# Kernel optimization log

Hardware: AMD Instinct MI355X
Metric: run time of the kernel (lower is better)

The kernel has to match this reference:

```python
import jax, jax.numpy as jnp
import numpy as np
import math

D_MODEL = 1024
N_HEADS = 16
FFN_DIM = 4096
B, L = 8, 1024
LN_EPS = 1e-5


def setup_inputs() -> dict:
    key = jax.random.key(0)
    ks = jax.random.split(key, 16)
    s = 1.0 / math.sqrt(D_MODEL)
    sf = 1.0 / math.sqrt(FFN_DIM)
    # weights stored [in, out] (transposed vs torch nn.Linear)
    return {
        "x": jax.random.normal(ks[0], (B, L, D_MODEL), dtype=jnp.float32),
        "Wq": jax.random.normal(ks[1], (D_MODEL, D_MODEL), dtype=jnp.float32) * s,
        "bq": jnp.zeros((D_MODEL,), jnp.float32),
        "Wk": jax.random.normal(ks[2], (D_MODEL, D_MODEL), dtype=jnp.float32) * s,
        "bk": jnp.zeros((D_MODEL,), jnp.float32),
        "Wv": jax.random.normal(ks[3], (D_MODEL, D_MODEL), dtype=jnp.float32) * s,
        "bv": jnp.zeros((D_MODEL,), jnp.float32),
        "Wo": jax.random.normal(ks[4], (D_MODEL, D_MODEL), dtype=jnp.float32) * s,
        "bo": jnp.zeros((D_MODEL,), jnp.float32),
        "W1": jax.random.normal(ks[5], (D_MODEL, FFN_DIM), dtype=jnp.float32) * s,
        "b1": jnp.zeros((FFN_DIM,), jnp.float32),
        "W2": jax.random.normal(ks[6], (FFN_DIM, D_MODEL), dtype=jnp.float32) * sf,
        "b2": jnp.zeros((D_MODEL,), jnp.float32),
        "gamma": jnp.ones((D_MODEL,), jnp.float32),
        "beta": jnp.zeros((D_MODEL,), jnp.float32),
    }


def reference(x, Wq, bq, Wk, bk, Wv, bv, Wo, bo, W1, b1, W2, b2, gamma, beta):
    Bb, Ll, D = x.shape
    H = N_HEADS
    E = D // H
    scale = 1.0 / math.sqrt(E)
    # multi-head attention (dropout is identity in eval)
    q = (x @ Wq + bq).reshape(Bb, Ll, H, E)
    k = (x @ Wk + bk).reshape(Bb, Ll, H, E)
    v = (x @ Wv + bv).reshape(Bb, Ll, H, E)
    scores = jnp.einsum('blhe,bshe->bhls', q, k)  # [B,H,L,L]
    A = jax.nn.softmax(scale * scores, axis=-1)
    ctx = jnp.einsum('bhls,bshd->blhd', A, v).reshape(Bb, Ll, D)
    attn_out = ctx @ Wo + bo
    x = x + attn_out
    # FFN: conv1d kernel_size=1 == pointwise linear; exact (erf) GELU as in F.gelu
    h = jax.nn.gelu(x @ W1 + b1, approximate=False)
    x = x + (h @ W2 + b2)
    # LayerNorm
    mu = jnp.mean(x, axis=-1, keepdims=True)
    var = jnp.mean(jnp.square(x - mu), axis=-1, keepdims=True)
    out = (x - mu) * jax.lax.rsqrt(var + LN_EPS) * gamma + beta
    return out
```

## Files before the change

### kernel.cpp

```cpp
#include <hip/hip_runtime.h>
#include <cmath>

typedef __attribute__((ext_vector_type(8))) _Float16 half8;
typedef __attribute__((ext_vector_type(4))) _Float16 half4;
typedef __attribute__((ext_vector_type(4))) float f32x4;

__device__ __forceinline__ void glds16(const void* g, void* l) {
  __builtin_amdgcn_global_load_lds(
      (__attribute__((address_space(1))) const void*)g,
      (__attribute__((address_space(3))) void*)l, 16, 0, 0);
}

__global__ __launch_bounds__(256) void k_cvt(const float* __restrict__ in,
                                             _Float16* __restrict__ out) {
  int i = (blockIdx.x * 256 + threadIdx.x) * 8;
  const f32x4* p = (const f32x4*)(in + i);
  f32x4 a = p[0], b = p[1];
  half8 h;
  h[0] = (_Float16)a[0]; h[1] = (_Float16)a[1]; h[2] = (_Float16)a[2]; h[3] = (_Float16)a[3];
  h[4] = (_Float16)b[0]; h[5] = (_Float16)b[1]; h[6] = (_Float16)b[2]; h[7] = (_Float16)b[3];
  *(half8*)(out + i) = h;
}

__global__ __launch_bounds__(256) void k_wt(const float* __restrict__ W,
                                            _Float16* __restrict__ Wt, int K, int N) {
  __shared__ float t[32][33];
  int x = threadIdx.x & 31, y4 = (threadIdx.x >> 5) << 2;
  int n0 = blockIdx.x << 5, k0 = blockIdx.y << 5;
#pragma unroll
  for (int r = 0; r < 4; ++r) t[y4 + r][x] = W[(size_t)(k0 + y4 + r) * N + n0 + x];
  __syncthreads();
#pragma unroll
  for (int r = 0; r < 4; ++r) Wt[(size_t)(n0 + y4 + r) * K + k0 + x] = (_Float16)t[x][y4 + r];
}

__global__ void k_biascat(const float* __restrict__ a, const float* __restrict__ b,
                          const float* __restrict__ c, float* __restrict__ o) {
  int i = blockIdx.x * 256 + threadIdx.x;
  const float* s = i < 1024 ? a : (i < 2048 ? b : c);
  o[i] = s[i & 1023];
}

template <int BM, int EPI>
__global__ __launch_bounds__(512, 2) void k_gemm8(
    const _Float16* __restrict__ A, const _Float16* __restrict__ Bt,
    const float* __restrict__ bias, const float* __restrict__ res,
    float* __restrict__ outf, _Float16* __restrict__ outh, int M, int N, int K) {
  constexpr int MR = BM / 32;
  constexpr int MH2 = MR / 2;
  constexpr int AL = BM * 64;
  constexpr int BL = 256 * 64;
  constexpr int ABYTES = BM * 128;
  constexpr int BBYTES = 256 * 128;
  constexpr int AB2 = 2 * ABYTES;
  __shared__ _Float16 lds[2 * (AL + BL)];
  const char* ldsc = (const char*)lds;

  const int tid = threadIdx.x;
  const int lane = tid & 63;
  const int w = tid >> 6, wr = w >> 2, wc = w & 3;
  const int l15 = lane & 15, grp = lane >> 4;

  const int gx = gridDim.x;
  const int nwg = gx * gridDim.y;
  const int lid = blockIdx.y * gx + blockIdx.x;
  const int wid = (lid & 7) * (nwg >> 3) + (lid >> 3);
  const int m0 = (wid / gx) * BM, n0 = (wid % gx) * 256;

  const int m2 = (l15 >> 2) & 1, m01 = l15 & 3;
  const int chunk0 = (m2 << 2) | (grp ^ m01);
  const int aoff0 = wr * 2048 + l15 * 128 + chunk0 * 16;
  const int aoff1 = aoff0 ^ 64;
  const int boff0 = wc * 2048 + l15 * 128 + chunk0 * 16;
  const int boff1 = boff0 ^ 64;

  const int srow = tid >> 3;
  const int scs8 = ((tid & 7) ^ (srow & 7)) * 8;
  const int NK = K >> 6;

  f32x4 acc[MR][4] = {};
  half8 af[MH2][2], bf[2][2];

#define STG_A(J, MHH, KN)                                                      \
  _Pragma("unroll") for (int s = 0; s < BM / 128; ++s)                         \
      glds16(A + (size_t)(m0 + (MHH) * (BM / 2) + s * 64 + srow) * K +         \
                 (size_t)(KN)*64 + scs8,                                       \
             lds + (J)*AL + ((MHH) * (BM / 2) + s * 64) * 64 + tid * 8);
#define STG_B(J, NHH, KN)                                                      \
  _Pragma("unroll") for (int s = 0; s < 2; ++s)                                \
      glds16(Bt + (size_t)(n0 + (NHH)*128 + s * 64 + srow) * K +               \
                  (size_t)(KN)*64 + scs8,                                      \
             lds + 2 * AL + (J)*BL + ((NHH)*128 + s * 64) * 64 + tid * 8);

#define VM_P1                                                                  \
  do {                                                                         \
    if constexpr (BM == 256) asm volatile("s_waitcnt vmcnt(4)" ::: "memory");  \
    else asm volatile("s_waitcnt vmcnt(2)" ::: "memory");                      \
  } while (0)
#define VM_P2                                                                  \
  do {                                                                         \
    if constexpr (BM == 256) asm volatile("s_waitcnt vmcnt(4)" ::: "memory");  \
    else asm volatile("s_waitcnt vmcnt(3)" ::: "memory");                      \
  } while (0)
#define VM_P3                                                                  \
  do {                                                                         \
    if constexpr (BM == 256) asm volatile("s_waitcnt vmcnt(4)" ::: "memory");  \
  } while (0)
#define VM_P4 VM_P2

#define PHASE(J, MHQ, NHQ, RA, RB, STGSTMT, VMSTMT)                            \
  {                                                                            \
    if constexpr (RA) {                                                        \
      _Pragma("unroll") for (int i = 0; i < MH2; ++i) {                        \
        af[i][0] = *(const half8*)(ldsc + (J)*ABYTES +                         \
                                   ((MHQ)*MH2 + i) * 4096 + aoff0);            \
        af[i][1] = *(const half8*)(ldsc + (J)*ABYTES +                         \
                                   ((MHQ)*MH2 + i) * 4096 + aoff1);            \
      }                                                                        \
    }                                                                          \
    if constexpr (RB) {                                                        \
      _Pragma("unroll") for (int n = 0; n < 2; ++n) {                          \
        bf[n][0] = *(const half8*)(ldsc + AB2 + (J)*BBYTES +                   \
                                   ((NHQ)*2 + n) * 8192 + boff0);              \
        bf[n][1] = *(const half8*)(ldsc + AB2 + (J)*BBYTES +                   \
                                   ((NHQ)*2 + n) * 8192 + boff1);              \
      }                                                                        \
    }                                                                          \
    STGSTMT;                                                                   \
    __builtin_amdgcn_s_barrier();                                              \
    asm volatile("s_waitcnt lgkmcnt(0)" ::: "memory");                         \
    __builtin_amdgcn_sched_barrier(0);                                         \
    __builtin_amdgcn_s_setprio(1);                                             \
    _Pragma("unroll") for (int ks = 0; ks < 2; ++ks)                           \
        _Pragma("unroll") for (int i = 0; i < MH2; ++i)                        \
            _Pragma("unroll") for (int n = 0; n < 2; ++n)                      \
                acc[(MHQ)*MH2 + i][(NHQ)*2 + n] =                              \
                    __builtin_amdgcn_mfma_f32_16x16x32_f16(                    \
                        af[i][ks], bf[n][ks], acc[(MHQ)*MH2 + i][(NHQ)*2 + n], \
                        0, 0, 0);                                              \
    __builtin_amdgcn_s_setprio(0);                                             \
    VMSTMT;                                                                    \
    __builtin_amdgcn_s_barrier();                                              \
  }

#define KTILE(J, KT)                                                           \
  {                                                                            \
    const int kn_ = ((KT) + 1 < NK) ? (KT) + 1 : (KT);                         \
    PHASE(J, 0, 0, true, true, STG_A(1 - (J), 0, kn_), VM_P1)                  \
    PHASE(J, 0, 1, false, true, STG_B(1 - (J), 0, kn_), VM_P2)                 \
    PHASE(J, 1, 1, true, false, STG_B(1 - (J), 1, kn_), VM_P3)                 \
    PHASE(J, 1, 0, false, true, STG_A(1 - (J), 1, kn_), VM_P4)                 \
  }

  STG_A(0, 0, 0) STG_B(0, 0, 0) STG_B(0, 1, 0) STG_A(0, 1, 0)
  if constexpr (BM == 256) asm volatile("s_waitcnt vmcnt(4)" ::: "memory");
  else asm volatile("s_waitcnt vmcnt(3)" ::: "memory");
  __builtin_amdgcn_s_barrier();

#pragma unroll 1
  for (int kt = 0; kt < NK; kt += 2) {
    KTILE(0, kt)
    KTILE(1, kt + 1)
  }
  asm volatile("s_waitcnt vmcnt(0)" ::: "memory");
#undef KTILE
#undef PHASE
#undef VM_P1
#undef VM_P2
#undef VM_P3
#undef VM_P4
#undef STG_A
#undef STG_B

  float bcol[4];
#pragma unroll
  for (int n = 0; n < 4; ++n) bcol[n] = bias[n0 + (n * 4 + wc) * 16 + l15];
#pragma unroll
  for (int m = 0; m < MR; ++m) {
#pragma unroll
    for (int rr = 0; rr < 4; ++rr) {
      const size_t row = m0 + (m * 2 + wr) * 16 + grp * 4 + rr;
#pragma unroll
      for (int n = 0; n < 4; ++n) {
        const int col = n0 + (n * 4 + wc) * 16 + l15;
        float v = acc[m][n][rr] + bcol[n];
        const size_t idx = row * N + col;
        if (EPI == 0) {
          outh[idx] = (_Float16)v;
        } else if (EPI == 1) {
          float t2 = v + res[idx];
          outf[idx] = t2;
          outh[idx] = (_Float16)t2;
        } else if (EPI == 2) {
          float g = 0.5f * v * (1.0f + erff(v * 0.70710678118654752f));
          outh[idx] = (_Float16)g;
        } else {
          outf[idx] = v + res[idx];
        }
      }
    }
  }
}

__global__ __launch_bounds__(256) void k_vt(const _Float16* __restrict__ qkv,
                                            _Float16* __restrict__ Vt) {
  __shared__ _Float16 t[64 * 66];
  const int tid = threadIdx.x;
  const int bh = blockIdx.y, b = bh >> 4, h = bh & 15;
  const int s0 = blockIdx.x << 6;
#pragma unroll
  for (int p = 0; p < 2; ++p) {
    int lin = p * 256 + tid;
    int s = lin >> 3, c8 = lin & 7;
    half8 v = *(const half8*)&qkv[(size_t)(b * 1024 + s0 + s) * 3072 + 2048 + h * 64 + c8 * 8];
    union { half8 h8; unsigned u[4]; } u;
    u.h8 = v;
    unsigned* d = (unsigned*)&t[s * 66 + c8 * 8];
#pragma unroll
    for (int k = 0; k < 4; ++k) d[k] = u.u[k];
  }
  __syncthreads();
#pragma unroll
  for (int p = 0; p < 2; ++p) {
    int lin = p * 256 + tid;
    int e = lin >> 3, c8 = lin & 7;
    half8 v;
#pragma unroll
    for (int j = 0; j < 8; ++j) v[j] = t[(c8 * 8 + j) * 66 + e];
    *(half8*)&Vt[(size_t)(bh * 64 + e) * 1024 + s0 + c8 * 8] = v;
  }
}

__global__ __launch_bounds__(256) void k_attn(const _Float16* __restrict__ qkv,
                                              const _Float16* __restrict__ Vt,
                                              _Float16* __restrict__ ctx) {
  __shared__ _Float16 Ks[128 * 64];
  __shared__ _Float16 Vs[64 * 128];
  __shared__ _Float16 Ps[4][16 * 136];
  const int tid = threadIdx.x;
  const int lane = tid & 63, w = tid >> 6;
  const int l15 = lane & 15, grp = lane >> 4;
  const int bh = blockIdx.y, b = bh >> 4, h = bh & 15;
  const int q0 = blockIdx.x << 6;
  const float CSC = 0.125f * 1.44269504088896f;

  half8 qf[2];
  {
    const _Float16* qp = qkv + (size_t)(b * 1024 + q0 + w * 16 + l15) * 3072 + h * 64 + grp * 8;
    qf[0] = *(const half8*)qp;
    qf[1] = *(const half8*)(qp + 32);
  }
  f32x4 octx[4] = {};
  float mrun = -1e30f, lrun = 0.f;

  for (int kt = 0; kt < 8; ++kt) {
    const int s0 = kt * 128;
#pragma unroll
    for (int i = 0; i < 4; ++i) {
      {
        int srow = i * 32 + (tid >> 3);
        int c8 = (tid & 7) ^ (srow & 7);
        glds16(qkv + (size_t)(b * 1024 + s0 + srow) * 3072 + 1024 + h * 64 + c8 * 8,
               Ks + w * 512 + i * 2048);
      }
      {
        int erow = i * 16 + (tid >> 4);
        int c16 = (tid & 15) ^ (erow & 7);
        glds16(Vt + (size_t)(bh * 64 + erow) * 1024 + s0 + c16 * 8,
               Vs + w * 512 + i * 2048);
      }
    }
    __syncthreads();
    f32x4 sacc[8] = {};
#pragma unroll
    for (int ks = 0; ks < 2; ++ks)
#pragma unroll
      for (int f = 0; f < 8; ++f) {
        int srow = f * 16 + l15;
        half8 kf = *(const half8*)&Ks[srow * 64 + ((ks * 32 + grp * 8) ^ ((srow & 7) * 8))];
        sacc[f] = __builtin_amdgcn_mfma_f32_16x16x32_f16(kf, qf[ks], sacc[f], 0, 0, 0);
      }
    float sv[8][4];
    float tmax = -1e30f;
#pragma unroll
    for (int f = 0; f < 8; ++f)
#pragma unroll
      for (int r = 0; r < 4; ++r) {
        float v = sacc[f][r] * CSC;
        sv[f][r] = v;
        tmax = fmaxf(tmax, v);
      }
    tmax = fmaxf(tmax, __shfl_xor(tmax, 16));
    tmax = fmaxf(tmax, __shfl_xor(tmax, 32));
    float mnew = fmaxf(mrun, tmax);
    float corr = exp2f(mrun - mnew);
    float tsum = 0.f;
#pragma unroll
    for (int f = 0; f < 8; ++f)
#pragma unroll
      for (int r = 0; r < 4; ++r) {
        float pv = exp2f(sv[f][r] - mnew);
        sv[f][r] = pv;
        tsum += pv;
      }
    tsum += __shfl_xor(tsum, 16);
    tsum += __shfl_xor(tsum, 32);
    lrun = lrun * corr + tsum;
    mrun = mnew;
#pragma unroll
    for (int r = 0; r < 4; ++r) {
      float cq = __shfl(corr, (lane & 48) + grp * 4 + r);
#pragma unroll
      for (int jf = 0; jf < 4; ++jf) octx[jf][r] *= cq;
    }
#pragma unroll
    for (int f = 0; f < 8; ++f) {
      half4 pk;
      pk[0] = (_Float16)sv[f][0]; pk[1] = (_Float16)sv[f][1];
      pk[2] = (_Float16)sv[f][2]; pk[3] = (_Float16)sv[f][3];
      *(half4*)&Ps[w][l15 * 136 + f * 16 + grp * 4] = pk;
    }
#pragma unroll
    for (int ks2 = 0; ks2 < 4; ++ks2) {
      half8 pa = *(const half8*)&Ps[w][l15 * 136 + ks2 * 32 + grp * 8];
#pragma unroll
      for (int jf = 0; jf < 4; ++jf) {
        int erow = jf * 16 + l15;
        half8 vb = *(const half8*)&Vs[erow * 128 + ((ks2 * 32 + grp * 8) ^ ((erow & 7) * 8))];
        octx[jf] = __builtin_amdgcn_mfma_f32_16x16x32_f16(pa, vb, octx[jf], 0, 0, 0);
      }
    }
    __syncthreads();
  }
#pragma unroll
  for (int r = 0; r < 4; ++r) {
    float lq = __shfl(lrun, (lane & 48) + grp * 4 + r);
    float inv = 1.0f / lq;
    const size_t row = b * 1024 + q0 + w * 16 + grp * 4 + r;
#pragma unroll
    for (int jf = 0; jf < 4; ++jf)
      ctx[row * 1024 + h * 64 + jf * 16 + l15] = (_Float16)(octx[jf][r] * inv);
  }
}

__global__ __launch_bounds__(256) void k_ln(const float* xin, const float* __restrict__ gamma,
                                            const float* __restrict__ beta, float* out) {
  __shared__ float red[8];
  const int tid = threadIdx.x;
  const size_t row = blockIdx.x;
  f32x4 v = *(const f32x4*)&xin[row * 1024 + tid * 4];
  float s = v[0] + v[1] + v[2] + v[3];
  float s2 = v[0] * v[0] + v[1] * v[1] + v[2] * v[2] + v[3] * v[3];
#pragma unroll
  for (int o = 32; o >= 1; o >>= 1) {
    s += __shfl_xor(s, o);
    s2 += __shfl_xor(s2, o);
  }
  if ((tid & 63) == 0) { red[tid >> 6] = s; red[4 + (tid >> 6)] = s2; }
  __syncthreads();
  s = red[0] + red[1] + red[2] + red[3];
  s2 = red[4] + red[5] + red[6] + red[7];
  float mu = s * (1.0f / 1024.0f);
  float var = s2 * (1.0f / 1024.0f) - mu * mu;
  float rs = rsqrtf(var + 1e-5f);
  f32x4 g = *(const f32x4*)&gamma[tid * 4];
  f32x4 bt = *(const f32x4*)&beta[tid * 4];
  f32x4 o4;
#pragma unroll
  for (int r = 0; r < 4; ++r) o4[r] = (v[r] - mu) * rs * g[r] + bt[r];
  *(f32x4*)&out[row * 1024 + tid * 4] = o4;
}

extern "C" void kernel_launch(void* const* d_in, const int* in_sizes, int n_in,
                              void* d_out, int out_size, void* d_ws, size_t ws_size,
                              hipStream_t stream) {
  (void)in_sizes; (void)n_in; (void)out_size; (void)ws_size;
  const float* x  = (const float*)d_in[0];
  const float* Wq = (const float*)d_in[1];  const float* bq = (const float*)d_in[2];
  const float* Wk = (const float*)d_in[3];  const float* bk = (const float*)d_in[4];
  const float* Wv = (const float*)d_in[5];  const float* bv = (const float*)d_in[6];
  const float* Wo = (const float*)d_in[7];  const float* bo = (const float*)d_in[8];
  const float* W1 = (const float*)d_in[9];  const float* b1 = (const float*)d_in[10];
  const float* W2 = (const float*)d_in[11]; const float* b2 = (const float*)d_in[12];
  const float* gamma = (const float*)d_in[13];
  const float* beta  = (const float*)d_in[14];
  float* out = (float*)d_out;

  char* p = (char*)d_ws;
  _Float16* xb    = (_Float16*)p;  p += (size_t)16 << 20;
  _Float16* qkv   = (_Float16*)p;
  _Float16* hbuf  = (_Float16*)p;  p += (size_t)48 << 20;
  _Float16* Vt    = (_Float16*)p;  p += (size_t)16 << 20;
  _Float16* Wqkvt = (_Float16*)p;  p += (size_t)3072 * 1024 * 2;
  _Float16* Wot   = (_Float16*)p;  p += (size_t)1024 * 1024 * 2;
  _Float16* W1t   = (_Float16*)p;  p += (size_t)4096 * 1024 * 2;
  _Float16* W2t   = (_Float16*)p;  p += (size_t)4096 * 1024 * 2;
  float*    bqkv  = (float*)p;     p += (size_t)3072 * 4;
  float*    x1    = (float*)p;     p += (size_t)32 << 20;
  _Float16* x1b   = (_Float16*)p;  p += (size_t)16 << 20;
  _Float16* ctx   = xb;

  k_cvt<<<4096, 256, 0, stream>>>(x, xb);
  k_wt<<<dim3(32, 32), 256, 0, stream>>>(Wq, Wqkvt, 1024, 1024);
  k_wt<<<dim3(32, 32), 256, 0, stream>>>(Wk, Wqkvt + 1024 * 1024, 1024, 1024);
  k_wt<<<dim3(32, 32), 256, 0, stream>>>(Wv, Wqkvt + 2048 * 1024, 1024, 1024);
  k_wt<<<dim3(32, 32), 256, 0, stream>>>(Wo, Wot, 1024, 1024);
  k_wt<<<dim3(128, 32), 256, 0, stream>>>(W1, W1t, 1024, 4096);
  k_wt<<<dim3(32, 128), 256, 0, stream>>>(W2, W2t, 4096, 1024);
  k_biascat<<<12, 256, 0, stream>>>(bq, bk, bv, bqkv);

  k_gemm8<128, 0><<<dim3(12, 64), 512, 0, stream>>>(xb, Wqkvt, bqkv, nullptr, nullptr, qkv,
                                                    8192, 3072, 1024);
  k_vt<<<dim3(16, 128), 256, 0, stream>>>(qkv, Vt);
  k_attn<<<dim3(16, 128), 256, 0, stream>>>(qkv, Vt, ctx);
  k_gemm8<128, 1><<<dim3(4, 64), 512, 0, stream>>>(ctx, Wot, bo, x, x1, x1b, 8192, 1024, 1024);
  k_gemm8<256, 2><<<dim3(16, 32), 512, 0, stream>>>(x1b, W1t, b1, nullptr, nullptr, hbuf,
                                                    8192, 4096, 1024);
  k_gemm8<128, 3><<<dim3(4, 64), 512, 0, stream>>>(hbuf, W2t, b2, x1, out, nullptr,
                                                   8192, 1024, 4096);
  k_ln<<<8192, 256, 0, stream>>>(out, gamma, beta, out);
}
```

Baseline: 382.3 us.

## Batch next-tile GEMM prefetch into one phase and use polynomial erf in GELU

All global-to-LDS loads for the next K tile are now issued together in the first MFMA phase, instead of being spread one slice per phase. The vmcnt waits are regrouped to match. The explicit lgkmcnt(0) wait and sched_barrier before each MFMA block are removed, so the compiler can interleave LDS reads with MFMAs. The GELU epilogue replaces erff with an Abramowitz-Stegun polynomial plus __expf, which cuts epilogue transcendental cost at a small accuracy cost. Issuing all loads at once may create bursty memory traffic and changes how latency hiding is distributed across phases.

```diff
diff --git a/kernel.cpp b/kernel.cpp
--- a/kernel.cpp
+++ b/kernel.cpp
@@ -9,6 +9,17 @@
   __builtin_amdgcn_global_load_lds(
       (__attribute__((address_space(1))) const void*)g,
       (__attribute__((address_space(3))) void*)l, 16, 0, 0);
+}
+
+__device__ __forceinline__ float fast_erf(float x) {
+  float ax = fabsf(x);
+  float t = 1.0f / (1.0f + 0.3275911f * ax);
+  float y = t * (0.254829592f +
+            t * (-0.284496736f +
+            t * (1.421413741f +
+            t * (-1.453152027f + t * 1.061405429f))));
+  float r = 1.0f - y * __expf(-ax * ax);
+  return copysignf(r, x);
 }
 
 __global__ __launch_bounds__(256) void k_cvt(const float* __restrict__ in,
@@ -92,21 +103,20 @@
                   (size_t)(KN)*64 + scs8,                                      \
              lds + 2 * AL + (J)*BL + ((NHH)*128 + s * 64) * 64 + tid * 8);
 
-#define VM_P1                                                                  \
+#define STG_ALL(J, KN)                                                         \
+  STG_A(J, 0, KN) STG_B(J, 0, KN) STG_B(J, 1, KN) STG_A(J, 1, KN)
+
+#define VM_A                                                                   \
   do {                                                                         \
-    if constexpr (BM == 256) asm volatile("s_waitcnt vmcnt(4)" ::: "memory");  \
-    else asm volatile("s_waitcnt vmcnt(2)" ::: "memory");                      \
+    if constexpr (BM == 256) asm volatile("s_waitcnt vmcnt(8)" ::: "memory");  \
+    else asm volatile("s_waitcnt vmcnt(6)" ::: "memory");                      \
   } while (0)
-#define VM_P2                                                                  \
+#define VM_B                                                                   \
   do {                                                                         \
     if constexpr (BM == 256) asm volatile("s_waitcnt vmcnt(4)" ::: "memory");  \
     else asm volatile("s_waitcnt vmcnt(3)" ::: "memory");                      \
   } while (0)
-#define VM_P3                                                                  \
-  do {                                                                         \
-    if constexpr (BM == 256) asm volatile("s_waitcnt vmcnt(4)" ::: "memory");  \
-  } while (0)
-#define VM_P4 VM_P2
+#define VM_NONE
 
 #define PHASE(J, MHQ, NHQ, RA, RB, STGSTMT, VMSTMT)                            \
   {                                                                            \
@@ -128,8 +138,6 @@
     }                                                                          \
     STGSTMT;                                                                   \
     __builtin_amdgcn_s_barrier();                                              \
-    asm volatile("s_waitcnt lgkmcnt(0)" ::: "memory");                         \
-    __builtin_amdgcn_sched_barrier(0);                                         \
     __builtin_amdgcn_s_setprio(1);                                             \
     _Pragma("unroll") for (int ks = 0; ks < 2; ++ks)                           \
         _Pragma("unroll") for (int i = 0; i < MH2; ++i)                        \
@@ -146,15 +154,14 @@
 #define KTILE(J, KT)                                                           \
   {                                                                            \
     const int kn_ = ((KT) + 1 < NK) ? (KT) + 1 : (KT);                         \
-    PHASE(J, 0, 0, true, true, STG_A(1 - (J), 0, kn_), VM_P1)                  \
-    PHASE(J, 0, 1, false, true, STG_B(1 - (J), 0, kn_), VM_P2)                 \
-    PHASE(J, 1, 1, true, false, STG_B(1 - (J), 1, kn_), VM_P3)                 \
-    PHASE(J, 1, 0, false, true, STG_A(1 - (J), 1, kn_), VM_P4)                 \
-  }
-
-  STG_A(0, 0, 0) STG_B(0, 0, 0) STG_B(0, 1, 0) STG_A(0, 1, 0)
-  if constexpr (BM == 256) asm volatile("s_waitcnt vmcnt(4)" ::: "memory");
-  else asm volatile("s_waitcnt vmcnt(3)" ::: "memory");
+    PHASE(J, 0, 0, true, true, STG_ALL(1 - (J), kn_), VM_A)                    \
+    PHASE(J, 0, 1, false, true, , VM_NONE)                                     \
+    PHASE(J, 1, 1, true, false, , VM_NONE)                                     \
+    PHASE(J, 1, 0, false, true, , VM_B)                                        \
+  }
+
+  STG_ALL(0, 0)
+  VM_B;
   __builtin_amdgcn_s_barrier();
 
 #pragma unroll 1
@@ -165,10 +172,10 @@
   asm volatile("s_waitcnt vmcnt(0)" ::: "memory");
 #undef KTILE
 #undef PHASE
-#undef VM_P1
-#undef VM_P2
-#undef VM_P3
-#undef VM_P4
+#undef VM_A
+#undef VM_B
+#undef VM_NONE
+#undef STG_ALL
 #undef STG_A
 #undef STG_B
 
@@ -192,7 +199,7 @@
           outf[idx] = t2;
           outh[idx] = (_Float16)t2;
         } else if (EPI == 2) {
-          float g = 0.5f * v * (1.0f + erff(v * 0.70710678118654752f));
+          float g = 0.5f * v * (1.0f + fast_erf(v * 0.70710678118654752f));
           outh[idx] = (_Float16)g;
         } else {
           outf[idx] = v + res[idx];
```

After: 380.0 us. Within noise of the previous version (-0.6%).
